# Optimization experiments

Hardware: AMD Instinct MI355X
Metric: run time of the kernel (lower is better)

## Reference

```python
import jax, jax.numpy as jnp
import numpy as np

EUCLTHRES = 0.02  # module default, meters
N_VERTS = 10475   # SMPL-X vertex count
BATCH = 2


def setup_inputs() -> dict:
    key = jax.random.key(0)
    k1, k2 = jax.random.split(key)
    vertices = jax.random.normal(k1, (BATCH, N_VERTS, 3), dtype=jnp.float32)
    # geodesic mask: True where geodesic distance >= geothres (most pairs)
    geomask = jax.random.randint(k2, (N_VERTS, N_VERTS), 0, 2) > 0
    # symmetrize like a real geodesic-distance-derived mask
    geomask = jnp.logical_or(geomask, geomask.T)
    return {"vertices": vertices, "geomask": geomask}


def reference(vertices, geomask):
    # batch_pairwise_dist (squared): ||x_i||^2 + ||x_j||^2 - 2 x_i . x_j
    sq = jnp.sum(vertices * vertices, axis=-1)                      # [B, N]
    dots = jnp.einsum('bnd,bmd->bnm', vertices, vertices)           # [B, N, N]
    v2v = sq[:, :, None] + sq[:, None, :] - 2.0 * dots              # [B, N, N]
    # v2v[:, ~geomask] = inf  (mask out geodesically-close pairs)
    v2v = jnp.where(geomask[None, :, :], v2v, jnp.inf)
    # torch.min(v2v, dim=1): min over first vertex index for each column j
    v2v_min = jnp.min(v2v, axis=1)                                  # [B, N]
    in_contact = v2v_min < EUCLTHRES ** 2                           # [B, N] bool
    return (v2v_min, in_contact)
```

## Files before the change

kernel.cpp:

```cpp
#include <hip/hip_runtime.h>
#include <math.h>


#define NV   10475
#define NB   2
#define BLK  256
#define CPB  1024
#define JB   ((NV + CPB - 1) / CPB)
#define CH   48
#define RC   ((NV + CH - 1) / CH)
#define RU   4

__device__ __forceinline__ float sq_nofma(float x, float y, float z) {
    return __fadd_rn(__fadd_rn(__fmul_rn(x, x), __fmul_rn(y, y)), __fmul_rn(z, z));
}

template <int CTRL>
__device__ __forceinline__ float dppmin(float v) {
    int s = __builtin_amdgcn_update_dpp(__float_as_int(v), __float_as_int(v),
                                        CTRL, 0xF, 0xF, false);
    return fminf(v, __int_as_float(s));
}

__device__ __forceinline__ float wave_min_to_lane63(float v) {
    v = dppmin<0x111>(v);
    v = dppmin<0x112>(v);
    v = dppmin<0x114>(v);
    v = dppmin<0x118>(v);
    v = dppmin<0x142>(v);
    v = dppmin<0x143>(v);
    return v;
}

__global__ __launch_bounds__(BLK) void sc_partial(
    const float* __restrict__ verts,
    const int*   __restrict__ gmask,
    float*       __restrict__ colpart,
    float*       __restrict__ rowpart)
{
    __shared__ float4 sv[CH * NB];
    __shared__ float  rmin[CH][4][NB];

    const int tid  = threadIdx.x;
    const int jb   = blockIdx.x;
    const int rcb  = blockIdx.y;
    const int j0   = jb * CPB;
    const int jmax = (j0 + CPB - 1 < NV - 1) ? (j0 + CPB - 1) : (NV - 1);
    const int r0   = rcb * CH;
    if (r0 > jmax) return;
    const int r1    = ((r0 + CH < jmax + 1) ? (r0 + CH) : (jmax + 1));
    const int nrows = r1 - r0;
    const int wv    = tid >> 6;

    for (int k = tid; k < nrows * NB; k += BLK) {
        int rr = k >> 1, b = k & 1;
        const float* vp = verts + ((size_t)b * NV + (r0 + rr)) * 3;
        float x = vp[0], y = vp[1], z = vp[2];
        sv[rr * NB + b] = make_float4(x, y, z, sq_nofma(x, y, z));
    }
    __syncthreads();

    int  cols[4];
    bool cval[4];
    float cx2[NB][4], cy2[NB][4], cz2[NB][4], cs[NB][4];
#pragma unroll
    for (int c = 0; c < 4; ++c) {
        int col = j0 + tid + c * BLK;
        cval[c] = (col < NV);
        cols[c] = cval[c] ? col : (NV - 1);
#pragma unroll
        for (int b = 0; b < NB; ++b) {
            const float* vp = verts + ((size_t)b * NV + cols[c]) * 3;
            float x = vp[0], y = vp[1], z = vp[2];
            cx2[b][c] = __fmul_rn(2.0f, x);
            cy2[b][c] = __fmul_rn(2.0f, y);
            cz2[b][c] = __fmul_rn(2.0f, z);
            cs[b][c]  = sq_nofma(x, y, z);
        }
    }

    float mn[NB][4];
#pragma unroll
    for (int b = 0; b < NB; ++b)
#pragma unroll
        for (int c = 0; c < 4; ++c) mn[b][c] = __builtin_inff();

#define ROW_BODY(ROWIDX, MK0, MK1, MK2, MK3)                                   \
    {                                                                          \
        int rr = (ROWIDX);                                                     \
        float4 a0 = sv[rr * NB + 0];                                           \
        float4 a1 = sv[rr * NB + 1];                                           \
        float rf0 = __builtin_inff(), rf1 = __builtin_inff();                  \
        int mks[4] = {MK0, MK1, MK2, MK3};                                     \
        _Pragma("unroll")                                                      \
        for (int c = 0; c < 4; ++c) {                                          \
            bool act = cval[c] && (mks[c] != 0);                               \
            float d0 = __fadd_rn(__fadd_rn(__fmul_rn(a0.x, cx2[0][c]),         \
                                           __fmul_rn(a0.y, cy2[0][c])),        \
                                 __fmul_rn(a0.z, cz2[0][c]));                  \
            float v0 = __fsub_rn(__fadd_rn(a0.w, cs[0][c]), d0);               \
            float t0 = act ? v0 : __builtin_inff();                            \
            mn[0][c] = fminf(mn[0][c], t0);                                    \
            rf0      = fminf(rf0, t0);                                         \
            float d1 = __fadd_rn(__fadd_rn(__fmul_rn(a1.x, cx2[1][c]),         \
                                           __fmul_rn(a1.y, cy2[1][c])),        \
                                 __fmul_rn(a1.z, cz2[1][c]));                  \
            float v1 = __fsub_rn(__fadd_rn(a1.w, cs[1][c]), d1);               \
            float t1 = act ? v1 : __builtin_inff();                            \
            mn[1][c] = fminf(mn[1][c], t1);                                    \
            rf1      = fminf(rf1, t1);                                         \
        }                                                                      \
        rf0 = wave_min_to_lane63(rf0);                                         \
        rf1 = wave_min_to_lane63(rf1);                                         \
        if ((tid & 63) == 63) {                                                \
            rmin[rr][wv][0] = rf0;                                             \
            rmin[rr][wv][1] = rf1;                                             \
        }                                                                      \
    }

    int i = r0;
    for (; i + RU <= r1; i += RU) {
        int mk[RU][4];
#pragma unroll
        for (int r = 0; r < RU; ++r) {
            const int* grow = gmask + (size_t)(i + r) * NV;
#pragma unroll
            for (int c = 0; c < 4; ++c) mk[r][c] = grow[cols[c]];
        }
#pragma unroll
        for (int r = 0; r < RU; ++r)
            ROW_BODY(i - r0 + r, mk[r][0], mk[r][1], mk[r][2], mk[r][3]);
    }
    for (; i < r1; ++i) {
        const int* grow = gmask + (size_t)i * NV;
        int m0 = grow[cols[0]], m1 = grow[cols[1]];
        int m2 = grow[cols[2]], m3 = grow[cols[3]];
        ROW_BODY(i - r0, m0, m1, m2, m3);
    }
#undef ROW_BODY

    __syncthreads();

    for (int k = tid; k < nrows * NB; k += BLK) {
        int rr = k >> 1, b = k & 1;
        float m = fminf(fminf(rmin[rr][0][b], rmin[rr][1][b]),
                        fminf(rmin[rr][2][b], rmin[rr][3][b]));
        rowpart[((size_t)jb * NB + b) * NV + (r0 + rr)] = m;
    }

#pragma unroll
    for (int c = 0; c < 4; ++c) {
        if (cval[c]) {
            colpart[((size_t)rcb * NB + 0) * NV + cols[c]] = mn[0][c];
            colpart[((size_t)rcb * NB + 1) * NV + cols[c]] = mn[1][c];
        }
    }
}

__global__ __launch_bounds__(BLK) void sc_reduce(
    const float* __restrict__ colpart,
    const float* __restrict__ rowpart,
    float*       __restrict__ out)
{
    int idx = blockIdx.x * BLK + threadIdx.x;
    if (idx >= NB * NV) return;
    int b = idx / NV, j = idx - b * NV;

    int jb    = j / CPB;
    int jmax  = ((jb + 1) * CPB - 1 < NV - 1) ? ((jb + 1) * CPB - 1) : (NV - 1);
    int rcmax = jmax / CH;

    float m = __builtin_inff();
    for (int rcb = 0; rcb <= rcmax; ++rcb)
        m = fminf(m, colpart[((size_t)rcb * NB + b) * NV + j]);
#pragma unroll
    for (int jb2 = 0; jb2 < JB; ++jb2)
        if (jb2 >= jb)
            m = fminf(m, rowpart[((size_t)jb2 * NB + b) * NV + j]);

    out[idx] = m;
    out[NB * NV + idx] = ((double)m < 0.02 * 0.02) ? 1.0f : 0.0f;
}

extern "C" void kernel_launch(void* const* d_in, const int* in_sizes, int n_in,
                              void* d_out, int out_size, void* d_ws, size_t ws_size,
                              hipStream_t stream) {
    const float* verts = (const float*)d_in[0];
    const int*   gmask = (const int*)d_in[1];
    float* out     = (float*)d_out;
    float* colpart = (float*)d_ws;
    float* rowpart = colpart + (size_t)RC * NB * NV;

    dim3 g1(JB, RC);
    sc_partial<<<g1, dim3(BLK), 0, stream>>>(verts, gmask, colpart, rowpart);

    int nred = (NB * NV + BLK - 1) / BLK;
    sc_reduce<<<nred, dim3(BLK), 0, stream>>>(colpart, rowpart, out);
}
```

Before: 591.4 us.

## Persistent compact tile grid with wider column tiles and pipelined mask loads

Replaces the 2D grid, which launched many blocks that exited early for tiles above the triangle, with a persistent grid of 644 blocks. These blocks walk an explicit list of 1288 valid triangular tiles. Each thread now covers 8 columns instead of 4 and row chunks drop to 32. Mask loads for the next row pair are software-pipelined ahead of compute. The intent is to remove wasted block launches, improve load balance and hide gmask latency. The cost is higher register pressure, bounded by launch_bounds of 3, and hardcoded tile counts tied to NV.

Result: slower. 1.705 ms (+188.4%).

```diff
diff --git a/kernel.cpp b/kernel.cpp
--- a/kernel.cpp
+++ b/kernel.cpp
@@ -5,11 +5,13 @@
 #define NV   10475
 #define NB   2
 #define BLK  256
-#define CPB  1024
+#define NC   8
+#define CPB  (BLK * NC)
 #define JB   ((NV + CPB - 1) / CPB)
-#define CH   48
-#define RC   ((NV + CH - 1) / CH)
-#define RU   4
+#define CH   32
+#define RCT  ((NV + CH - 1) / CH)
+#define NTILES 1288
+#define NBLK   644
 
 __device__ __forceinline__ float sq_nofma(float x, float y, float z) {
     return __fadd_rn(__fadd_rn(__fmul_rn(x, x), __fmul_rn(y, y)), __fmul_rn(z, z));
@@ -32,7 +34,7 @@
     return v;
 }
 
-__global__ __launch_bounds__(BLK) void sc_partial(
+__global__ __launch_bounds__(BLK, 3) void sc_partial(
     const float* __restrict__ verts,
     const int*   __restrict__ gmask,
     float*       __restrict__ colpart,
@@ -41,118 +43,136 @@
     __shared__ float4 sv[CH * NB];
     __shared__ float  rmin[CH][4][NB];
 
-    const int tid  = threadIdx.x;
-    const int jb   = blockIdx.x;
-    const int rcb  = blockIdx.y;
-    const int j0   = jb * CPB;
-    const int jmax = (j0 + CPB - 1 < NV - 1) ? (j0 + CPB - 1) : (NV - 1);
-    const int r0   = rcb * CH;
-    if (r0 > jmax) return;
-    const int r1    = ((r0 + CH < jmax + 1) ? (r0 + CH) : (jmax + 1));
-    const int nrows = r1 - r0;
-    const int wv    = tid >> 6;
-
-    for (int k = tid; k < nrows * NB; k += BLK) {
-        int rr = k >> 1, b = k & 1;
-        const float* vp = verts + ((size_t)b * NV + (r0 + rr)) * 3;
-        float x = vp[0], y = vp[1], z = vp[2];
-        sv[rr * NB + b] = make_float4(x, y, z, sq_nofma(x, y, z));
-    }
-    __syncthreads();
-
-    int  cols[4];
-    bool cval[4];
-    float cx2[NB][4], cy2[NB][4], cz2[NB][4], cs[NB][4];
-#pragma unroll
-    for (int c = 0; c < 4; ++c) {
-        int col = j0 + tid + c * BLK;
-        cval[c] = (col < NV);
-        cols[c] = cval[c] ? col : (NV - 1);
-#pragma unroll
-        for (int b = 0; b < NB; ++b) {
-            const float* vp = verts + ((size_t)b * NV + cols[c]) * 3;
+    const int tid = threadIdx.x;
+    const int wv  = tid >> 6;
+
+    for (int t = blockIdx.x; t < NTILES; t += NBLK) {
+        int jb, rcb;
+        if      (t <  64) { jb = 0; rcb = t;       }
+        else if (t < 192) { jb = 1; rcb = t -  64; }
+        else if (t < 384) { jb = 2; rcb = t - 192; }
+        else if (t < 640) { jb = 3; rcb = t - 384; }
+        else if (t < 960) { jb = 4; rcb = t - 640; }
+        else              { jb = 5; rcb = t - 960; }
+
+        const int j0    = jb * CPB;
+        const int jmax  = (j0 + CPB - 1 < NV - 1) ? (j0 + CPB - 1) : (NV - 1);
+        const int r0    = rcb * CH;
+        const int nrows = (CH < jmax + 1 - r0) ? CH : (jmax + 1 - r0);
+        const int nr4   = (nrows + 3) & ~3;
+
+        __syncthreads();
+
+        for (int k = tid; k < nr4 * NB; k += BLK) {
+            int rr = k >> 1, b = k & 1;
+            int row = r0 + rr; if (row > jmax) row = jmax;
+            const float* vp = verts + ((size_t)b * NV + row) * 3;
             float x = vp[0], y = vp[1], z = vp[2];
-            cx2[b][c] = __fmul_rn(2.0f, x);
-            cy2[b][c] = __fmul_rn(2.0f, y);
-            cz2[b][c] = __fmul_rn(2.0f, z);
-            cs[b][c]  = sq_nofma(x, y, z);
-        }
-    }
-
-    float mn[NB][4];
-#pragma unroll
-    for (int b = 0; b < NB; ++b)
-#pragma unroll
-        for (int c = 0; c < 4; ++c) mn[b][c] = __builtin_inff();
-
-#define ROW_BODY(ROWIDX, MK0, MK1, MK2, MK3)                                   \
-    {                                                                          \
-        int rr = (ROWIDX);                                                     \
-        float4 a0 = sv[rr * NB + 0];                                           \
-        float4 a1 = sv[rr * NB + 1];                                           \
-        float rf0 = __builtin_inff(), rf1 = __builtin_inff();                  \
-        int mks[4] = {MK0, MK1, MK2, MK3};                                     \
-        _Pragma("unroll")                                                      \
-        for (int c = 0; c < 4; ++c) {                                          \
-            bool act = cval[c] && (mks[c] != 0);                               \
-            float d0 = __fadd_rn(__fadd_rn(__fmul_rn(a0.x, cx2[0][c]),         \
-                                           __fmul_rn(a0.y, cy2[0][c])),        \
-                                 __fmul_rn(a0.z, cz2[0][c]));                  \
-            float v0 = __fsub_rn(__fadd_rn(a0.w, cs[0][c]), d0);               \
-            float t0 = act ? v0 : __builtin_inff();                            \
-            mn[0][c] = fminf(mn[0][c], t0);                                    \
-            rf0      = fminf(rf0, t0);                                         \
-            float d1 = __fadd_rn(__fadd_rn(__fmul_rn(a1.x, cx2[1][c]),         \
-                                           __fmul_rn(a1.y, cy2[1][c])),        \
-                                 __fmul_rn(a1.z, cz2[1][c]));                  \
-            float v1 = __fsub_rn(__fadd_rn(a1.w, cs[1][c]), d1);               \
-            float t1 = act ? v1 : __builtin_inff();                            \
-            mn[1][c] = fminf(mn[1][c], t1);                                    \
-            rf1      = fminf(rf1, t1);                                         \
-        }                                                                      \
-        rf0 = wave_min_to_lane63(rf0);                                         \
-        rf1 = wave_min_to_lane63(rf1);                                         \
-        if ((tid & 63) == 63) {                                                \
-            rmin[rr][wv][0] = rf0;                                             \
-            rmin[rr][wv][1] = rf1;                                             \
-        }                                                                      \
-    }
-
-    int i = r0;
-    for (; i + RU <= r1; i += RU) {
-        int mk[RU][4];
-#pragma unroll
-        for (int r = 0; r < RU; ++r) {
-            const int* grow = gmask + (size_t)(i + r) * NV;
-#pragma unroll
-            for (int c = 0; c < 4; ++c) mk[r][c] = grow[cols[c]];
-        }
-#pragma unroll
-        for (int r = 0; r < RU; ++r)
-            ROW_BODY(i - r0 + r, mk[r][0], mk[r][1], mk[r][2], mk[r][3]);
-    }
-    for (; i < r1; ++i) {
-        const int* grow = gmask + (size_t)i * NV;
-        int m0 = grow[cols[0]], m1 = grow[cols[1]];
-        int m2 = grow[cols[2]], m3 = grow[cols[3]];
-        ROW_BODY(i - r0, m0, m1, m2, m3);
-    }
+            sv[rr * NB + b] = make_float4(x, y, z, sq_nofma(x, y, z));
+        }
+        __syncthreads();
+
+        int  cols[NC];
+        bool cval[NC];
+        float cx2[NB][NC], cy2[NB][NC], cz2[NB][NC], cs[NB][NC];
+#pragma unroll
+        for (int c = 0; c < NC; ++c) {
+            int col = j0 + tid + c * BLK;
+            cval[c] = (col < NV);
+            cols[c] = cval[c] ? col : (NV - 1);
+#pragma unroll
+            for (int b = 0; b < NB; ++b) {
+                const float* vp = verts + ((size_t)b * NV + cols[c]) * 3;
+                float x = vp[0], y = vp[1], z = vp[2];
+                cx2[b][c] = __fmul_rn(2.0f, x);
+                cy2[b][c] = __fmul_rn(2.0f, y);
+                cz2[b][c] = __fmul_rn(2.0f, z);
+                cs[b][c]  = sq_nofma(x, y, z);
+            }
+        }
+
+        float mn[NB][NC];
+#pragma unroll
+        for (int b = 0; b < NB; ++b)
+#pragma unroll
+            for (int c = 0; c < NC; ++c) mn[b][c] = __builtin_inff();
+
+#define LOADP(LR, MK)                                                          \
+        {                                                                      \
+            int rA = r0 + (LR);     if (rA > jmax) rA = jmax;                  \
+            int rB = r0 + (LR) + 1; if (rB > jmax) rB = jmax;                  \
+            const int* gA = gmask + (size_t)rA * NV;                           \
+            const int* gB = gmask + (size_t)rB * NV;                           \
+            _Pragma("unroll")                                                  \
+            for (int c = 0; c < NC; ++c) MK[0][c] = gA[cols[c]];               \
+            _Pragma("unroll")                                                  \
+            for (int c = 0; c < NC; ++c) MK[1][c] = gB[cols[c]];               \
+        }
+
+#define ROW_BODY(LR, MKR)                                                      \
+        {                                                                      \
+            int lrr = (LR);                                                    \
+            float4 a0 = sv[lrr * NB + 0];                                      \
+            float4 a1 = sv[lrr * NB + 1];                                      \
+            float rf0 = __builtin_inff(), rf1 = __builtin_inff();              \
+            float t0[NC], t1[NC];                                              \
+            _Pragma("unroll")                                                  \
+            for (int c = 0; c < NC; ++c) {                                     \
+                bool act = cval[c] && (MKR[c] != 0);                           \
+                float d0 = __fadd_rn(__fadd_rn(__fmul_rn(a0.x, cx2[0][c]),     \
+                                               __fmul_rn(a0.y, cy2[0][c])),   \
+                                     __fmul_rn(a0.z, cz2[0][c]));              \
+                float v0 = __fsub_rn(__fadd_rn(a0.w, cs[0][c]), d0);           \
+                t0[c] = act ? v0 : __builtin_inff();                           \
+                mn[0][c] = fminf(mn[0][c], t0[c]);                             \
+                float d1 = __fadd_rn(__fadd_rn(__fmul_rn(a1.x, cx2[1][c]),     \
+                                               __fmul_rn(a1.y, cy2[1][c])),   \
+                                     __fmul_rn(a1.z, cz2[1][c]));              \
+                float v1 = __fsub_rn(__fadd_rn(a1.w, cs[1][c]), d1);           \
+                t1[c] = act ? v1 : __builtin_inff();                           \
+                mn[1][c] = fminf(mn[1][c], t1[c]);                             \
+            }                                                                  \
+            _Pragma("unroll")                                                  \
+            for (int c = 0; c < NC; c += 2) {                                  \
+                rf0 = fminf(rf0, fminf(t0[c], t0[c + 1]));         \
+                rf1 = fminf(rf1, fminf(t1[c], t1[c + 1]));                     \
+            }                                                                  \
+            rf0 = wave_min_to_lane63(rf0);                                     \
+            rf1 = wave_min_to_lane63(rf1);                                     \
+            if ((tid & 63) == 63) {                                            \
+                rmin[lrr][wv][0] = rf0;                                        \
+                rmin[lrr][wv][1] = rf1;                                        \
+            }                                                                  \
+        }
+
+        int mk0[2][NC], mk1[2][NC];
+        LOADP(0, mk0);
+        for (int lr = 0; lr < nr4; lr += 4) {
+            LOADP(lr + 2, mk1);
+            ROW_BODY(lr,     mk0[0]);
+            ROW_BODY(lr + 1, mk0[1]);
+            if (lr + 4 < nr4) LOADP(lr + 4, mk0);
+            ROW_BODY(lr + 2, mk1[0]);
+            ROW_BODY(lr + 3, mk1[1]);
+        }
+#undef LOADP
 #undef ROW_BODY
 
-    __syncthreads();
-
-    for (int k = tid; k < nrows * NB; k += BLK) {
-        int rr = k >> 1, b = k & 1;
-        float m = fminf(fminf(rmin[rr][0][b], rmin[rr][1][b]),
-                        fminf(rmin[rr][2][b], rmin[rr][3][b]));
-        rowpart[((size_t)jb * NB + b) * NV + (r0 + rr)] = m;
-    }
-
-#pragma unroll
-    for (int c = 0; c < 4; ++c) {
-        if (cval[c]) {
-            colpart[((size_t)rcb * NB + 0) * NV + cols[c]] = mn[0][c];
-            colpart[((size_t)rcb * NB + 1) * NV + cols[c]] = mn[1][c];
+        __syncthreads();
+
+        for (int k = tid; k < nrows * NB; k += BLK) {
+            int rr = k >> 1, b = k & 1;
+            float m = fminf(fminf(rmin[rr][0][b], rmin[rr][1][b]),
+                            fminf(rmin[rr][2][b], rmin[rr][3][b]));
+            rowpart[((size_t)jb * NB + b) * NV + (r0 + rr)] = m;
+        }
+
+#pragma unroll
+        for (int c = 0; c < NC; ++c) {
+            if (cval[c]) {
+                colpart[((size_t)rcb * NB + 0) * NV + cols[c]] = mn[0][c];
+                colpart[((size_t)rcb * NB + 1) * NV + cols[c]] = mn[1][c];
+            }
         }
     }
 }
@@ -171,6 +191,7 @@
     int rcmax = jmax / CH;
 
     float m = __builtin_inff();
+#pragma unroll 8
     for (int rcb = 0; rcb <= rcmax; ++rcb)
         m = fminf(m, colpart[((size_t)rcb * NB + b) * NV + j]);
 #pragma unroll
@@ -189,10 +210,9 @@
     const int*   gmask = (const int*)d_in[1];
     float* out     = (float*)d_out;
     float* colpart = (float*)d_ws;
-    float* rowpart = colpart + (size_t)RC * NB * NV;
-
-    dim3 g1(JB, RC);
-    sc_partial<<<g1, dim3(BLK), 0, stream>>>(verts, gmask, colpart, rowpart);
+    float* rowpart = colpart + (size_t)RCT * NB * NV;
+
+    sc_partial<<<NBLK, dim3(BLK), 0, stream>>>(verts, gmask, colpart, rowpart);
 
     int nred = (NB * NV + BLK - 1) / BLK;
     sc_reduce<<<nred, dim3(BLK), 0, stream>>>(colpart, rowpart, out);
```
